# Kernel optimization log

Hardware: AMD Instinct MI355X
Metric: run time of the kernel (lower is better)

Reference implementation:

```python
import jax, jax.numpy as jnp
import numpy as np

NUM_USERS = 200000
NUM_ARTISTS = 50000
LATENT_DIM = 64
NUM_EDGES = 2000000
NUM_LAYERS = 3


def setup_inputs() -> dict:
    key = jax.random.key(0)
    k_u, k_a, k_src, k_dst = jax.random.split(key, 4)
    x_users = jax.random.normal(k_u, (NUM_USERS, LATENT_DIM), dtype=jnp.float32)
    x_artists = jax.random.normal(k_a, (NUM_ARTISTS, LATENT_DIM), dtype=jnp.float32)
    # a2u: row 0 = artist (source) ids, row 1 = user (target) ids
    art = jax.random.randint(k_src, (NUM_EDGES,), 0, NUM_ARTISTS, dtype=jnp.int32)
    usr = jax.random.randint(k_dst, (NUM_EDGES,), 0, NUM_USERS, dtype=jnp.int32)
    edge_index_a2u = jnp.stack([art, usr], axis=0)
    # u2a is the reversed edge list: row 0 = user (source), row 1 = artist (target)
    edge_index_u2a = jnp.stack([usr, art], axis=0)
    return {
        "x_users": x_users,
        "x_artists": x_artists,
        "edge_index_a2u": edge_index_a2u,
        "edge_index_u2a": edge_index_u2a,
    }


def _scatter_mean(src_nodes, edge_index, dim_size):
    """Gather src_nodes[edge_index[0]] and scatter-mean onto edge_index[1].

    Matches torch_scatter.scatter(reduce='mean'): empty segments yield 0.
    """
    msgs = src_nodes[edge_index[0]]                     # [E, D] gather
    sums = jax.ops.segment_sum(msgs, edge_index[1], num_segments=dim_size)
    ones = jnp.ones((edge_index.shape[1],), dtype=src_nodes.dtype)
    counts = jax.ops.segment_sum(ones, edge_index[1], num_segments=dim_size)
    return sums / jnp.maximum(counts, 1.0)[:, None]


def reference(x_users, x_artists, edge_index_a2u, edge_index_u2a):
    scale = 1.0 / (NUM_LAYERS + 1)
    final_u = x_users * scale
    final_a = x_artists * scale
    for _ in range(NUM_LAYERS):
        x_users = _scatter_mean(x_artists, edge_index_a2u, NUM_USERS)
        x_artists = _scatter_mean(x_users, edge_index_u2a, NUM_ARTISTS)
        final_u = final_u + x_users * scale
        final_a = final_a + x_artists * scale
    return final_u, final_a
```

## Files before the change

kernel.cpp:

```cpp
#include <hip/hip_runtime.h>
#include <hip/hip_fp16.h>

#define D 64
#define TB 256

#define BSHIFT_U 10
#define BSHIFT_A 8
#define CAP    12288
#define CAPC_U 16384
#define CAPC_A 12288
#define TSHIFT 14
#define PCHUNK 2048

typedef _Float16 half8 __attribute__((ext_vector_type(8)));
typedef float float8 __attribute__((ext_vector_type(8)));
typedef float f32x4 __attribute__((ext_vector_type(4)));

__device__ __forceinline__ float8 h8_to_f8(half8 h) {
    return __builtin_convertvector(h, float8);
}
template <typename T>
__device__ __forceinline__ T ntl(const T* p) { return __builtin_nontemporal_load(p); }
template <typename T>
__device__ __forceinline__ void nts(T* p, T v) { __builtin_nontemporal_store(v, p); }

__global__ __launch_bounds__(TB) void cvt_f16_kernel(const f32x4* __restrict__ in,
                                                     half8* __restrict__ out, int n8) {
    int i = blockIdx.x * blockDim.x + threadIdx.x;
    int stride = gridDim.x * blockDim.x;
    for (int j = i; j < n8; j += stride) {
        f32x4 a = in[j * 2 + 0];
        f32x4 b = in[j * 2 + 1];
        half8 h;
        h[0] = (_Float16)a[0]; h[1] = (_Float16)a[1]; h[2] = (_Float16)a[2]; h[3] = (_Float16)a[3];
        h[4] = (_Float16)b[0]; h[5] = (_Float16)b[1]; h[6] = (_Float16)b[2]; h[7] = (_Float16)b[3];
        out[j] = h;
    }
}

struct PartShared {
    unsigned sorted[PCHUNK];
    unsigned short loc[PCHUNK];
    int cnt[256];
    int gbase[256];
    int seg[256];
    int scanbuf[TB];
};

__global__ __launch_bounds__(TB) void partition_both_kernel(const int* __restrict__ art,
                                                            const int* __restrict__ usr, int E,
                                                            int* __restrict__ bcur_u,
                                                            int* __restrict__ bcur_a,
                                                            unsigned* __restrict__ part_u,
                                                            unsigned* __restrict__ part_a,
                                                            int NBu, int NBa) {
    __shared__ PartShared sh;
    const int tid = threadIdx.x;
    const int dir = blockIdx.x & 1;
    const int c0 = (blockIdx.x >> 1) * PCHUNK;
    if (c0 >= E) return;
    const int m = min(PCHUNK, E - c0);
    const int NB = dir ? NBa : NBu;
    const int BSH = dir ? BSHIFT_A : BSHIFT_U;
    const int* key = dir ? art : usr;
    int* bcur = dir ? bcur_a : bcur_u;
    unsigned* part = dir ? part_a : part_u;

    for (int i = tid; i < NB; i += TB) sh.cnt[i] = 0;
    __syncthreads();
    for (int i = tid; i < m; i += TB) {
        int b = key[c0 + i] >> BSH;
        sh.loc[i] = (unsigned short)atomicAdd(&sh.cnt[b], 1);
    }
    __syncthreads();
    int v = (tid < NB) ? sh.cnt[tid] : 0;
    sh.scanbuf[tid] = v;
    __syncthreads();
    for (int off = 1; off < TB; off <<= 1) {
        int t = (tid >= off) ? sh.scanbuf[tid - off] : 0;
        __syncthreads();
        if (tid >= off) sh.scanbuf[tid] += t;
        __syncthreads();
    }
    if (tid < NB) {
        sh.seg[tid] = sh.scanbuf[tid] - v;
        if (v) sh.gbase[tid] = atomicAdd(&bcur[tid], v);
    }
    __syncthreads();
    const unsigned mask = (1u << BSH) - 1u;
    for (int i = tid; i < m; i += TB) {
        int a = art[c0 + i], u = usr[c0 + i];
        int k = dir ? a : u;
        int s = dir ? u : a;
        int b = k >> BSH;
        sh.sorted[sh.seg[b] + sh.loc[i]] = ((unsigned)s << BSH) | ((unsigned)k & mask);
    }
    __syncthreads();
    const int wid = tid >> 6;
    const int lane = tid & 63;
    for (int b = wid; b < NB; b += TB / 64) {
        int s = sh.seg[b];
        int send = (b + 1 < NB) ? sh.seg[b + 1] : m;
        if (send <= s) continue;
        unsigned* dst = part + (size_t)b * CAP + sh.gbase[b];
        for (int i = s + lane; i < send; i += 64) dst[i - s] = sh.sorted[i];
    }
}

template <int NPB, int NB, int BSHIFT>
__device__ __forceinline__ void local_csr_body(const unsigned* __restrict__ part,
                                               int ecount, int ebeg_p, int ebeg_c, int n0,
                                               int2* __restrict__ rowdeg,
                                               int* __restrict__ csr, int N,
                                               int* cnt, int* sdata) {
    const int tid = threadIdx.x;
    const int NBINS = NPB * NB;
    const int eend = ebeg_p + ecount;
    const unsigned mask = (unsigned)(NPB - 1);
    for (int i = tid; i < NBINS; i += TB) cnt[i] = 0;
    __syncthreads();
    for (int e = ebeg_p + tid; e < eend; e += TB) {
        unsigned r = part[e];
        int bin = (int)(r & mask) * NB + (int)((r >> BSHIFT) >> TSHIFT);
        atomicAdd(&cnt[bin], 1);
    }
    __syncthreads();
    const int ITEMS = NBINS / TB;
    const int NPT = ITEMS / NB;
    const int ib = tid * ITEMS;
    int dj[NPT], pdj[NPT], nsj[NPT];
    int local = 0;
    for (int j = 0; j < NPT; ++j) {
        int d = 0;
        for (int k = 0; k < NB; ++k) d += cnt[ib + j * NB + k];
        dj[j] = d;
        pdj[j] = (d + 3) & ~3;
        local += pdj[j];
    }
    sdata[tid] = local;
    __syncthreads();
    for (int off = 1; off < TB; off <<= 1) {
        int t = (tid >= off) ? sdata[tid - off] : 0;
        __syncthreads();
        if (tid >= off) sdata[tid] += t;
        __syncthreads();
    }
    int run = sdata[tid] - local;
    for (int j = 0; j < NPT; ++j) {
        nsj[j] = run;
        int c = run;
        for (int k = 0; k < NB; ++k) {
            int idx = ib + j * NB + k;
            int v = cnt[idx];
            cnt[idx] = c;
            c += v;
        }
        int n = n0 + tid * NPT + j;
        if (n < N) rowdeg[n] = make_int2(ebeg_c + run, dj[j]);
        run += pdj[j];
    }
    __syncthreads();
    for (int e = ebeg_p + tid; e < eend; e += TB) {
        unsigned r = part[e];
        int bin = (int)(r & mask) * NB + (int)((r >> BSHIFT) >> TSHIFT);
        int pos = atomicAdd(&cnt[bin], 1);
        csr[ebeg_c + pos] = (int)(r >> BSHIFT);
    }
    for (int j = 0; j < NPT; ++j)
        for (int k = dj[j]; k < pdj[j]; ++k) csr[ebeg_c + nsj[j] + k] = 0;
}

__global__ __launch_bounds__(TB) void local_csr_both_kernel(const unsigned* __restrict__ part_u,
                                                            const unsigned* __restrict__ part_a,
                                                            const int* __restrict__ bcur_u,
                                                            const int* __restrict__ bcur_a,
                                                            int2* __restrict__ rowdeg_u,
                                                            int2* __restrict__ rowdeg_a,
                                                            int* __restrict__ csr_u,
                                                            int* __restrict__ csr_a,
                                                            int NU, int NA, int NBu) {
    __shared__ int cnt[4096];
    __shared__ int sdata[TB];
    const int b = blockIdx.x;
    if (b < NBu) {
        local_csr_body<1024, 4, BSHIFT_U>(part_u, bcur_u[b], b * CAP, b * CAPC_U,
                                          b << BSHIFT_U, rowdeg_u, csr_u, NU, cnt, sdata);
    } else {
        const int bb = b - NBu;
        local_csr_body<256, 16, BSHIFT_A>(part_a, bcur_a[bb], bb * CAP, bb * CAPC_A,
                                          bb << BSHIFT_A, rowdeg_a, csr_a, NA, cnt, sdata);
    }
}

__global__ __launch_bounds__(TB) void gather_mean_kernel(const half8* __restrict__ src,
                                                         const int* __restrict__ csr,
                                                         const int2* __restrict__ rowdeg,
                                                         half8* __restrict__ x_out,
                                                         f32x4* __restrict__ final_acc,
                                                         const f32x4* __restrict__ init_src,
                                                         const f32x4* __restrict__ fin_in0,
                                                         const half8* __restrict__ fin_x1,
                                                         const half8* __restrict__ fin_x2,
                                                         f32x4* __restrict__ fin_out,
                                                         int N, float scale) {
    const int lane = threadIdx.x & 7;
    int g = (blockIdx.x * blockDim.x + threadIdx.x) >> 3;
    const int ngroups = (gridDim.x * blockDim.x) >> 3;
    const float8 r0 = h8_to_f8(src[lane]);
    for (int n = g; n < N; n += ngroups) {
        const long long rdl = ntl((const long long*)&rowdeg[n]);
        const int beg = (int)(unsigned)(rdl & 0xFFFFFFFFll);
        const int dg  = (int)(rdl >> 32);
        const int pd = (dg + 3) & ~3;
        const int end = beg + pd;
        float8 a0 = 0.f, a1 = 0.f, a2 = 0.f, a3 = 0.f;
        int e = beg;
        for (; e + 8 <= end; e += 8) {
            const int s0 = ntl(&csr[e + 0]);
            const int s1 = ntl(&csr[e + 1]);
            const int s2 = ntl(&csr[e + 2]);
            const int s3 = ntl(&csr[e + 3]);
            const int s4 = ntl(&csr[e + 4]);
            const int s5 = ntl(&csr[e + 5]);
            const int s6 = ntl(&csr[e + 6]);
            const int s7 = ntl(&csr[e + 7]);
            const half8 v0 = src[s0 * 8 + lane];
            const half8 v1 = src[s1 * 8 + lane];
            const half8 v2 = src[s2 * 8 + lane];
            const half8 v3 = src[s3 * 8 + lane];
            const half8 v4 = src[s4 * 8 + lane];
            const half8 v5 = src[s5 * 8 + lane];
            const half8 v6 = src[s6 * 8 + lane];
            const half8 v7 = src[s7 * 8 + lane];
            a0 += h8_to_f8(v0);
            a1 += h8_to_f8(v1);
            a2 += h8_to_f8(v2);
            a3 += h8_to_f8(v3);
            a0 += h8_to_f8(v4);
            a1 += h8_to_f8(v5);
            a2 += h8_to_f8(v6);
            a3 += h8_to_f8(v7);
        }
        if (e < end) {
            const int s0 = ntl(&csr[e + 0]);
            const int s1 = ntl(&csr[e + 1]);
            const int s2 = ntl(&csr[e + 2]);
            const int s3 = ntl(&csr[e + 3]);
            a0 += h8_to_f8(src[s0 * 8 + lane]);
            a1 += h8_to_f8(src[s1 * 8 + lane]);
            a2 += h8_to_f8(src[s2 * 8 + lane]);
            a3 += h8_to_f8(src[s3 * 8 + lane]);
        }
        float8 s = (a0 + a1) + (a2 + a3);
        s -= (float)(pd - dg) * r0;
        const float inv = 1.f / (float)(dg > 0 ? dg : 1);
        float8 x = s * inv;
        const int o8 = n * 8 + lane;
        if (x_out != nullptr) {
            half8 h;
            for (int k = 0; k < 8; ++k) h[k] = (_Float16)x[k];
            x_out[o8] = h;
        }
        const int fo = n * (D / 4) + lane * 2;
        if (fin_out != nullptr) {
            float8 t = h8_to_f8(ntl(&fin_x1[o8])) + h8_to_f8(ntl(&fin_x2[o8])) + x;
            f32x4 f0 = ntl(&fin_in0[fo + 0]);
            f32x4 f1 = ntl(&fin_in0[fo + 1]);
            f32x4 t0 = {t[0], t[1], t[2], t[3]};
            f32x4 t1 = {t[4], t[5], t[6], t[7]};
            nts(&fin_out[fo + 0], (f0 + t0) * scale);
            nts(&fin_out[fo + 1], (f1 + t1) * scale);
        }
        if (final_acc != nullptr) {
            f32x4 f0, f1;
            if (init_src != nullptr) {
                f0 = init_src[fo + 0] * scale;
                f1 = init_src[fo + 1] * scale;
            } else {
                f0 = final_acc[fo + 0];
                f1 = final_acc[fo + 1];
            }
            f32x4 x0 = {x[0], x[1], x[2], x[3]};
            f32x4 x1 = {x[4], x[5], x[6], x[7]};
            final_acc[fo + 0] = f0 + x0 * scale;
            final_acc[fo + 1] = f1 + x1 * scale;
        }
    }
}

extern "C" void kernel_launch(void* const* d_in, const int* in_sizes, int n_in,
                              void* d_out, int out_size, void* d_ws, size_t ws_size,
                              hipStream_t stream) {
    const float* x_users   = (const float*)d_in[0];
    const float* x_artists = (const float*)d_in[1];
    const int*   a2u       = (const int*)d_in[2];

    const int NU = in_sizes[0] / D;
    const int NA = in_sizes[1] / D;
    const int E  = in_sizes[2] / 2;
    const int* art = a2u;
    const int* usr = a2u + E;

    const float scale = 0.25f;

    const int NBu = (NU + (1 << BSHIFT_U) - 1) >> BSHIFT_U;
    const int NBa = (NA + (1 << BSHIFT_A) - 1) >> BSHIFT_A;

    char* w = (char*)d_ws;
    size_t off = 0;
    auto alloc = [&](size_t bytes) -> char* {
        char* p = w + off;
        off += (bytes + 255) & ~(size_t)255;
        return p;
    };
    int2* rowdeg_u = (int2*)alloc((size_t)NU * 8);
    int2* rowdeg_a = (int2*)alloc((size_t)NA * 8);
    int* bcur      = (int*)alloc((size_t)(NBu + NBa) * 4);
    int* bcur_u    = bcur;
    int* bcur_a    = bcur + NBu;
    int* csr_u     = (int*)alloc((size_t)NBu * CAPC_U * 4);
    int* csr_a     = (int*)alloc((size_t)NBa * CAPC_A * 4);
    half8* xa_in   = (half8*)alloc((size_t)NA * D * 2);
    unsigned* part_u = (unsigned*)alloc((size_t)NBu * CAP * 4);
    unsigned* part_a = (unsigned*)alloc((size_t)NBa * CAP * 4);

    const size_t XU = (size_t)NU * D * 2;
    const size_t XA = (size_t)NA * D * 2;
    const size_t XUa = (XU + 255) & ~(size_t)255;
    const size_t XAa = (XA + 255) & ~(size_t)255;

    const bool modeA = (off + 3 * XUa) <= ws_size;

    half8* x_u1 = (half8*)alloc(XU);
    half8* x_u2 = modeA ? (half8*)alloc(XU) : x_u1;
    half8* x_u3 = modeA ? (half8*)alloc(XU) : x_u1;
    char* part_base = (char*)part_u;
    half8* x_a1 = (half8*)(part_base);
    half8* x_a2 = modeA ? (half8*)(part_base + XAa) : x_a1;

    float* out_u = (float*)d_out;
    float* out_a = out_u + (size_t)NU * D;

    hipMemsetAsync(bcur, 0, (size_t)(NBu + NBa) * 4, stream);
    cvt_f16_kernel<<<1024, TB, 0, stream>>>((const f32x4*)x_artists, xa_in, NA * D / 8);
    const int nchunks = (E + PCHUNK - 1) / PCHUNK;
    partition_both_kernel<<<2 * nchunks, TB, 0, stream>>>(art, usr, E, bcur_u, bcur_a,
                                                          part_u, part_a, NBu, NBa);
    local_csr_both_kernel<<<NBu + NBa, TB, 0, stream>>>(part_u, part_a, bcur_u, bcur_a,
                                                        rowdeg_u, rowdeg_a,
                                                        csr_u, csr_a, NU, NA, NBu);

    half8* xu_buf[3] = {x_u1, x_u2, x_u3};
    half8* xa_buf[2] = {x_a1, x_a2};
    const half8* srcA = xa_in;
    for (int l = 0; l < 3; ++l) {
        const bool last = (l == 2);
        gather_mean_kernel<<<4096, TB, 0, stream>>>(
            srcA, csr_u, rowdeg_u, xu_buf[l],
            modeA ? nullptr : (f32x4*)out_u,
            (!modeA && l == 0) ? (const f32x4*)x_users : nullptr,
            (modeA && last) ? (const f32x4*)x_users : nullptr,
            (modeA && last) ? x_u1 : nullptr,
            (modeA && last) ? x_u2 : nullptr,
            (modeA && last) ? (f32x4*)out_u : nullptr,
            NU, scale);
        gather_mean_kernel<<<2048, TB, 0, stream>>>(
            xu_buf[l], csr_a, rowdeg_a,
            (modeA && last) ? nullptr : (modeA ? xa_buf[l] : x_a1),
            modeA ? nullptr : (f32x4*)out_a,
            (!modeA && l == 0) ? (const f32x4*)x_artists : nullptr,
            (modeA && last) ? (const f32x4*)x_artists : nullptr,
            (modeA && last) ? x_a1 : nullptr,
            (modeA && last) ? x_a2 : nullptr,
            (modeA && last) ? (f32x4*)out_a : nullptr,
            NA, scale);
        srcA = modeA ? xa_buf[l < 2 ? l : 0] : x_a1;
    }
}
```

Baseline: 385.9 us.

## Shard partition bucket cursors to cut global atomic contention

Splits each bucket's global cursor into 8 shards picked by chunk index, so partition blocks spread their atomicAdds over more addresses. Each shard gets its own capacity slice, and the local CSR build walks all shards. This trades less contention on the global atomics for more loops and a tighter per-shard capacity, which could overflow if edges are distributed unevenly. The gather kernel also switches from nontemporal to normal loads for the csr and rowdeg reads.

New measurement: 350.8 us. 1.1x faster.

```diff
diff --git a/kernel.cpp b/kernel.cpp
--- a/kernel.cpp
+++ b/kernel.cpp
@@ -6,7 +6,9 @@
 
 #define BSHIFT_U 10
 #define BSHIFT_A 8
-#define CAP    12288
+#define SHARDS 8
+#define SCAP   1536
+#define CAP    (SHARDS * SCAP)
 #define CAPC_U 16384
 #define CAPC_A 12288
 #define TSHIFT 14
@@ -57,7 +59,9 @@
     __shared__ PartShared sh;
     const int tid = threadIdx.x;
     const int dir = blockIdx.x & 1;
-    const int c0 = (blockIdx.x >> 1) * PCHUNK;
+    const int cidx = blockIdx.x >> 1;
+    const int shard = cidx & (SHARDS - 1);
+    const int c0 = cidx * PCHUNK;
     if (c0 >= E) return;
     const int m = min(PCHUNK, E - c0);
     const int NB = dir ? NBa : NBu;
@@ -84,7 +88,10 @@
     }
     if (tid < NB) {
         sh.seg[tid] = sh.scanbuf[tid] - v;
-        if (v) sh.gbase[tid] = atomicAdd(&bcur[tid], v);
+        if (v) {
+            int old = atomicAdd(&bcur[tid * SHARDS + shard], v);
+            sh.gbase[tid] = tid * CAP + shard * SCAP + old;
+        }
     }
     __syncthreads();
     const unsigned mask = (1u << BSH) - 1u;
@@ -102,27 +109,33 @@
         int s = sh.seg[b];
         int send = (b + 1 < NB) ? sh.seg[b + 1] : m;
         if (send <= s) continue;
-        unsigned* dst = part + (size_t)b * CAP + sh.gbase[b];
+        unsigned* dst = part + (size_t)sh.gbase[b];
         for (int i = s + lane; i < send; i += 64) dst[i - s] = sh.sorted[i];
     }
 }
 
 template <int NPB, int NB, int BSHIFT>
 __device__ __forceinline__ void local_csr_body(const unsigned* __restrict__ part,
-                                               int ecount, int ebeg_p, int ebeg_c, int n0,
+                                               const int* __restrict__ shard_cnt,
+                                               int ebeg_p, int ebeg_c, int n0,
                                                int2* __restrict__ rowdeg,
                                                int* __restrict__ csr, int N,
                                                int* cnt, int* sdata) {
     const int tid = threadIdx.x;
     const int NBINS = NPB * NB;
-    const int eend = ebeg_p + ecount;
     const unsigned mask = (unsigned)(NPB - 1);
+    int cs[SHARDS];
+    for (int s = 0; s < SHARDS; ++s) cs[s] = shard_cnt[s];
     for (int i = tid; i < NBINS; i += TB) cnt[i] = 0;
     __syncthreads();
-    for (int e = ebeg_p + tid; e < eend; e += TB) {
-        unsigned r = part[e];
-        int bin = (int)(r & mask) * NB + (int)((r >> BSHIFT) >> TSHIFT);
-        atomicAdd(&cnt[bin], 1);
+    for (int s = 0; s < SHARDS; ++s) {
+        const int base = ebeg_p + s * SCAP;
+        const int endv = base + cs[s];
+        for (int e = base + tid; e < endv; e += TB) {
+            unsigned r = part[e];
+            int bin = (int)(r & mask) * NB + (int)((r >> BSHIFT) >> TSHIFT);
+            atomicAdd(&cnt[bin], 1);
+        }
     }
     __syncthreads();
     const int ITEMS = NBINS / TB;
@@ -160,11 +173,15 @@
         run += pdj[j];
     }
     __syncthreads();
-    for (int e = ebeg_p + tid; e < eend; e += TB) {
-        unsigned r = part[e];
-        int bin = (int)(r & mask) * NB + (int)((r >> BSHIFT) >> TSHIFT);
-        int pos = atomicAdd(&cnt[bin], 1);
-        csr[ebeg_c + pos] = (int)(r >> BSHIFT);
+    for (int s = 0; s < SHARDS; ++s) {
+        const int base = ebeg_p + s * SCAP;
+        const int endv = base + cs[s];
+        for (int e = base + tid; e < endv; e += TB) {
+            unsigned r = part[e];
+            int bin = (int)(r & mask) * NB + (int)((r >> BSHIFT) >> TSHIFT);
+            int pos = atomicAdd(&cnt[bin], 1);
+            csr[ebeg_c + pos] = (int)(r >> BSHIFT);
+        }
     }
     for (int j = 0; j < NPT; ++j)
         for (int k = dj[j]; k < pdj[j]; ++k) csr[ebeg_c + nsj[j] + k] = 0;
@@ -183,11 +200,11 @@
     __shared__ int sdata[TB];
     const int b = blockIdx.x;
     if (b < NBu) {
-        local_csr_body<1024, 4, BSHIFT_U>(part_u, bcur_u[b], b * CAP, b * CAPC_U,
+        local_csr_body<1024, 4, BSHIFT_U>(part_u, bcur_u + b * SHARDS, b * CAP, b * CAPC_U,
                                           b << BSHIFT_U, rowdeg_u, csr_u, NU, cnt, sdata);
     } else {
         const int bb = b - NBu;
-        local_csr_body<256, 16, BSHIFT_A>(part_a, bcur_a[bb], bb * CAP, bb * CAPC_A,
+        local_csr_body<256, 16, BSHIFT_A>(part_a, bcur_a + bb * SHARDS, bb * CAP, bb * CAPC_A,
                                           bb << BSHIFT_A, rowdeg_a, csr_a, NA, cnt, sdata);
     }
 }
@@ -208,22 +225,22 @@
     const int ngroups = (gridDim.x * blockDim.x) >> 3;
     const float8 r0 = h8_to_f8(src[lane]);
     for (int n = g; n < N; n += ngroups) {
-        const long long rdl = ntl((const long long*)&rowdeg[n]);
-        const int beg = (int)(unsigned)(rdl & 0xFFFFFFFFll);
-        const int dg  = (int)(rdl >> 32);
+        const int2 rd = rowdeg[n];
+        const int beg = rd.x;
+        const int dg = rd.y;
         const int pd = (dg + 3) & ~3;
         const int end = beg + pd;
         float8 a0 = 0.f, a1 = 0.f, a2 = 0.f, a3 = 0.f;
         int e = beg;
         for (; e + 8 <= end; e += 8) {
-            const int s0 = ntl(&csr[e + 0]);
-            const int s1 = ntl(&csr[e + 1]);
-            const int s2 = ntl(&csr[e + 2]);
-            const int s3 = ntl(&csr[e + 3]);
-            const int s4 = ntl(&csr[e + 4]);
-            const int s5 = ntl(&csr[e + 5]);
-            const int s6 = ntl(&csr[e + 6]);
-            const int s7 = ntl(&csr[e + 7]);
+            const int s0 = csr[e + 0];
+            const int s1 = csr[e + 1];
+            const int s2 = csr[e + 2];
+            const int s3 = csr[e + 3];
+            const int s4 = csr[e + 4];
+            const int s5 = csr[e + 5];
+            const int s6 = csr[e + 6];
+            const int s7 = csr[e + 7];
             const half8 v0 = src[s0 * 8 + lane];
             const half8 v1 = src[s1 * 8 + lane];
             const half8 v2 = src[s2 * 8 + lane];
@@ -242,10 +259,10 @@
             a3 += h8_to_f8(v7);
         }
         if (e < end) {
-            const int s0 = ntl(&csr[e + 0]);
-            const int s1 = ntl(&csr[e + 1]);
-            const int s2 = ntl(&csr[e + 2]);
-            const int s3 = ntl(&csr[e + 3]);
+            const int s0 = csr[e + 0];
+            const int s1 = csr[e + 1];
+            const int s2 = csr[e + 2];
+            const int s3 = csr[e + 3];
             a0 += h8_to_f8(src[s0 * 8 + lane]);
             a1 += h8_to_f8(src[s1 * 8 + lane]);
             a2 += h8_to_f8(src[s2 * 8 + lane]);
@@ -315,9 +332,9 @@
     };
     int2* rowdeg_u = (int2*)alloc((size_t)NU * 8);
     int2* rowdeg_a = (int2*)alloc((size_t)NA * 8);
-    int* bcur      = (int*)alloc((size_t)(NBu + NBa) * 4);
+    int* bcur      = (int*)alloc((size_t)(NBu + NBa) * SHARDS * 4);
     int* bcur_u    = bcur;
-    int* bcur_a    = bcur + NBu;
+    int* bcur_a    = bcur + NBu * SHARDS;
     int* csr_u     = (int*)alloc((size_t)NBu * CAPC_U * 4);
     int* csr_a     = (int*)alloc((size_t)NBa * CAPC_A * 4);
     half8* xa_in   = (half8*)alloc((size_t)NA * D * 2);
@@ -341,7 +358,7 @@
     float* out_u = (float*)d_out;
     float* out_a = out_u + (size_t)NU * D;
 
-    hipMemsetAsync(bcur, 0, (size_t)(NBu + NBa) * 4, stream);
+    hipMemsetAsync(bcur, 0, (size_t)(NBu + NBa) * SHARDS * 4, stream);
     cvt_f16_kernel<<<1024, TB, 0, stream>>>((const f32x4*)x_artists, xa_in, NA * D / 8);
     const int nchunks = (E + PCHUNK - 1) / PCHUNK;
     partition_both_kernel<<<2 * nchunks, TB, 0, stream>>>(art, usr, E, bcur_u, bcur_a,
```
